# Performance work log

Measured on AMD Instinct MI355X. Metric: run time of the kernel, lower is better.

## Reference

```python
import jax, jax.numpy as jnp
import numpy as np

B, D = 8192, 1024

def setup_inputs() -> dict:
    key = jax.random.key(0)
    ks = jax.random.split(key, 5)
    scale = 1.0 / np.sqrt(D)
    return {
        "x": jax.random.normal(ks[0], (B, D), dtype=jnp.float32),
        "h": jax.random.normal(ks[1], (B, D), dtype=jnp.float32),
        "c": jax.random.normal(ks[2], (B, D), dtype=jnp.float32),
        # gate order: [input, forget, output, candidate]
        "Wx": jax.random.normal(ks[3], (4, D, D), dtype=jnp.float32) * scale,
        "Wh": jax.random.normal(ks[4], (4, D, D), dtype=jnp.float32) * scale,
    }

def reference(x, h, c, Wx, Wh):
    # two batched GEMMs covering all 8 projections: [B,D] x [4,D,D] -> [4,B,D]
    gx = jnp.einsum('bd,gdk->gbk', x, Wx)
    gh = jnp.einsum('bd,gdk->gbk', h, Wh)
    g = gx + gh
    i = jax.nn.sigmoid(g[0])
    f = jax.nn.sigmoid(g[1])
    o = jax.nn.sigmoid(g[2])
    u = jnp.tanh(g[3])
    c_t = i * u + f * c
    h_t = o * jnp.tanh(c_t)
    return (h_t, c_t)
```

## Files before the change

### kernel.cpp

```cpp
#include <hip/hip_runtime.h>
#include <hip/hip_bf16.h>
#include <cstdint>


#define LDS_TOTAL 131072

typedef __attribute__((ext_vector_type(8))) short bf16x8;
typedef __attribute__((ext_vector_type(16))) float f32x16;
typedef __attribute__((ext_vector_type(4))) unsigned int u32x4;

static __device__ __forceinline__ unsigned short f2bf(float f) {
  union { float f; unsigned int u; } v; v.f = f;
  unsigned int u = v.u;
  unsigned int r = (u + 0x7FFFu + ((u >> 16) & 1u)) >> 16;
  return (unsigned short)r;
}

static __device__ __forceinline__ void load16(const void* gp, void* lp) {
  __builtin_amdgcn_global_load_lds(
      (const __attribute__((address_space(1))) void*)gp,
      (__attribute__((address_space(3))) void*)lp, 16, 0, 0);
}

static __device__ __forceinline__ float sigmoid_f(float x) {
  return 1.0f / (1.0f + __expf(-x));
}
static __device__ __forceinline__ float tanh_f(float x) {
  float e = __expf(-2.0f * fabsf(x));
  float r = (1.0f - e) / (1.0f + e);
  return copysignf(r, x);
}

__global__ __launch_bounds__(256) void pack_a_kernel(
    const float* __restrict__ x, const float* __restrict__ h,
    unsigned short* __restrict__ Ap) {
  __shared__ float tile[64][65];
  const int b0 = (blockIdx.x >> 5) << 6;
  const int k0 = (blockIdx.x & 31) << 6;
  const float* src; int ks;
  if (k0 < 1024) { src = x; ks = k0; } else { src = h; ks = k0 - 1024; }
  const int r = threadIdx.x >> 4;
  const int c4 = (threadIdx.x & 15) << 2;
  #pragma unroll
  for (int s = 0; s < 4; ++s) {
    float4 v = *(const float4*)(src + (size_t)(b0 + s * 16 + r) * 1024 + ks + c4);
    tile[s * 16 + r][c4 + 0] = v.x; tile[s * 16 + r][c4 + 1] = v.y;
    tile[s * 16 + r][c4 + 2] = v.z; tile[s * 16 + r][c4 + 3] = v.w;
  }
  __syncthreads();
  #pragma unroll
  for (int i = 0; i < 2; ++i) {
    int cc = i * 256 + threadIdx.x;
    int kb = cc >> 6, bb = cc & 63;
    union { unsigned short s[8]; u32x4 v; } o;
    #pragma unroll
    for (int e = 0; e < 8; ++e) o.s[e] = f2bf(tile[bb][kb * 8 + e]);
    *(u32x4*)(Ap + ((size_t)((k0 >> 3) + kb) * 8192 + b0 + bb) * 8) = o.v;
  }
}

__global__ __launch_bounds__(256) void prep_w_kernel(
    const float* __restrict__ Wx, const float* __restrict__ Wh,
    unsigned short* __restrict__ Wt2) {
  __shared__ float tile[64][65];
  const int g = blockIdx.x >> 9;
  const int kt = (blockIdx.x >> 4) & 31;
  const int nt = blockIdx.x & 15;
  const int k0 = kt << 6, n0 = nt << 6;
  const float* W; int ks;
  if (k0 < 1024) { W = Wx + (size_t)g * 1048576; ks = k0; }
  else           { W = Wh + (size_t)g * 1048576; ks = k0 - 1024; }
  const int r = threadIdx.x >> 4;
  const int c4 = (threadIdx.x & 15) << 2;
  #pragma unroll
  for (int s = 0; s < 4; ++s) {
    float4 v = *(const float4*)(W + (size_t)(ks + s * 16 + r) * 1024 + n0 + c4);
    tile[s * 16 + r][c4 + 0] = v.x; tile[s * 16 + r][c4 + 1] = v.y;
    tile[s * 16 + r][c4 + 2] = v.z; tile[s * 16 + r][c4 + 3] = v.w;
  }
  __syncthreads();
  #pragma unroll
  for (int i = 0; i < 2; ++i) {
    int cc = i * 256 + threadIdx.x;
    int kb = cc >> 6, nn = cc & 63;
    union { unsigned short s[8]; u32x4 v; } o;
    #pragma unroll
    for (int e = 0; e < 8; ++e) o.s[e] = f2bf(tile[kb * 8 + e][nn]);
    *(u32x4*)(Wt2 + ((size_t)((k0 >> 3) + kb) * 4096 + g * 1024 + n0 + nn) * 8) = o.v;
  }
}

#define VMW(n) asm volatile("s_waitcnt vmcnt(" #n ")" ::: "memory")
#define LGKM0() asm volatile("s_waitcnt lgkmcnt(0)" ::: "memory")
#define BAR() __builtin_amdgcn_s_barrier()

__global__ __launch_bounds__(512, 2) void lstm_gemm_kernel(
    const unsigned short* __restrict__ Ap,
    const unsigned short* __restrict__ Wt2,
    const float* __restrict__ cprev,
    float* __restrict__ out) {
  extern __shared__ char lds[];
  const int tid = threadIdx.x;
  const int l = tid & 63;
  const int w = tid >> 6;
  const int wr = w >> 1;
  const int wc = w & 1;
  const int bid = blockIdx.x;
  const int xcd = bid & 7;
  const int cc = bid >> 3;
  const int nt = xcd * 2 + (cc >> 5);
  const int mt = cc & 31;
  const int m0 = mt << 8;
  const int n0 = nt << 6;

  char* const buf0 = lds;
  char* const buf1 = lds + 65536;

  f32x16 acc[2][4];
  #pragma unroll
  for (int mf = 0; mf < 2; ++mf)
    #pragma unroll
    for (int g = 0; g < 4; ++g) acc[mf][g] = (f32x16)0.0f;

  const int ln = l & 31;
  const int hl = l >> 5;

  const int aBase = hl * 4096 + (wr * 64 + ln) * 16;
  const int bBase = 32768 + hl * 1024 + (wc * 32 + ln) * 16;

  const unsigned short* const gA =
      Ap + (size_t)(tid >> 8) * 65536 + (size_t)(m0 + (tid & 255)) * 8;
  const unsigned short* const gB =
      Wt2 + (size_t)((tid >> 6) & 1) * 32768 +
      (size_t)((tid >> 7) * 1024 + n0 + (tid & 63)) * 8;
  const int dA = (tid & ~63) << 4;
  const int dB = 32768 + ((tid & ~63) << 4);

  auto stPair = [&](char* buf, int j, int t) {
    load16(gA + (size_t)(t * 8 + j * 2) * 65536, buf + j * 8192 + dA);
    load16(gB + (size_t)(t * 8 + j * 2) * 32768, buf + j * 8192 + dB);
  };

  bf16x8 a_[2][2], b_[2][4];
  auto rd2 = [&](const char* bufc, int h) {
    #pragma unroll
    for (int r = 0; r < 2; ++r) {
      const char* pb = bufc + (2 * h + r) * 8192;
      a_[r][0] = *(const bf16x8*)(pb + aBase);
      a_[r][1] = *(const bf16x8*)(pb + aBase + 512);
      b_[r][0] = *(const bf16x8*)(pb + bBase);
      b_[r][1] = *(const bf16x8*)(pb + bBase + 2048);
      b_[r][2] = *(const bf16x8*)(pb + bBase + 4096);
      b_[r][3] = *(const bf16x8*)(pb + bBase + 6144);
    }
  };
  auto mfma2 = [&]() {
    __builtin_amdgcn_s_setprio(1);
    #pragma unroll
    for (int r = 0; r < 2; ++r)
      #pragma unroll
      for (int mf = 0; mf < 2; ++mf)
        #pragma unroll
        for (int g = 0; g < 4; ++g)
          acc[mf][g] = __builtin_amdgcn_mfma_f32_32x32x16_bf16(
              a_[r][mf], b_[r][g], acc[mf][g], 0, 0, 0);
    __builtin_amdgcn_s_setprio(0);
  };

  #pragma unroll
  for (int j = 0; j < 4; ++j) stPair(buf0, j, 0);
  stPair(buf1, 0, 1); stPair(buf1, 1, 1);
  VMW(4);
  BAR();

  #pragma unroll 1
  for (int t = 0; t < 30; ++t) {
    char* bufc = lds + ((t & 1) << 16);
    char* bufn = lds + (((t + 1) & 1) << 16);
    rd2(bufc, 0);
    stPair(bufn, 2, t + 1); stPair(bufn, 3, t + 1);
    VMW(8); BAR(); LGKM0();
    mfma2();
    BAR();
    rd2(bufc, 1);
    stPair(bufc, 0, t + 2); stPair(bufc, 1, t + 2);
    VMW(8); BAR(); LGKM0();
    mfma2();
    BAR();
  }
  rd2(buf0, 0); stPair(buf1, 2, 31); stPair(buf1, 3, 31);
  VMW(8); BAR(); LGKM0(); mfma2(); BAR();
  rd2(buf0, 1);
  VMW(4); BAR(); LGKM0(); mfma2(); BAR();
  rd2(buf1, 0);
  VMW(0); BAR(); LGKM0(); mfma2(); BAR();
  rd2(buf1, 1);
  LGKM0(); mfma2();

  const int colB = n0 + wc * 32 + ln;
  #pragma unroll
  for (int mf = 0; mf < 2; ++mf) {
    #pragma unroll
    for (int r = 0; r < 16; ++r) {
      int row = m0 + wr * 64 + mf * 32 + (r & 3) + ((r >> 2) << 3) + (hl << 2);
      float gi = acc[mf][0][r];
      float gf = acc[mf][1][r];
      float go = acc[mf][2][r];
      float gu = acc[mf][3][r];
      float i_ = sigmoid_f(gi);
      float f_ = sigmoid_f(gf);
      float o_ = sigmoid_f(go);
      float u_ = tanh_f(gu);
      size_t idx = (size_t)row * 1024 + colB;
      float ct = i_ * u_ + f_ * cprev[idx];
      float ht = o_ * tanh_f(ct);
      out[idx] = ht;
      out[8388608 + idx] = ct;
    }
  }
}

extern "C" void kernel_launch(void* const* d_in, const int* in_sizes, int n_in,
                              void* d_out, int out_size, void* d_ws, size_t ws_size,
                              hipStream_t stream) {
  const float* x  = (const float*)d_in[0];
  const float* h  = (const float*)d_in[1];
  const float* c  = (const float*)d_in[2];
  const float* Wx = (const float*)d_in[3];
  const float* Wh = (const float*)d_in[4];
  float* out = (float*)d_out;

  unsigned short* Ap  = (unsigned short*)d_ws;
  unsigned short* Wt2 = (unsigned short*)((char*)d_ws + 33554432);

  hipFuncSetAttribute((const void*)lstm_gemm_kernel,
                      hipFuncAttributeMaxDynamicSharedMemorySize, LDS_TOTAL);

  pack_a_kernel<<<4096, 256, 0, stream>>>(x, h, Ap);
  prep_w_kernel<<<2048, 256, 0, stream>>>(Wx, Wh, Wt2);
  lstm_gemm_kernel<<<dim3(512), dim3(512), LDS_TOTAL, stream>>>(Ap, Wt2, c, out);
}
```

Before: 167.5 us.

## Fuse activation fp32-to-bf16 packing into GEMM mainloop, drop pack kernel

Removes the separate pack_a_kernel, which converted x and h to a bf16 K-blocked layout in workspace. The GEMM kernel now loads fp32 rows of x/h directly into registers, converts them to bf16 and writes them to LDS after the MFMA phase. This pipelines the register loads alongside the async B loads. It saves a full read and write pass over the 64MB of activations. In exchange the GEMM reads A as fp32, so A traffic doubles, and each M-tile's A is re-read by all 16 N-tile blocks. It also adds VALU conversion work, register pressure and possible LDS write bank conflicts in the mainloop.

```diff
diff --git a/kernel.cpp b/kernel.cpp
--- a/kernel.cpp
+++ b/kernel.cpp
@@ -29,34 +29,6 @@
   float e = __expf(-2.0f * fabsf(x));
   float r = (1.0f - e) / (1.0f + e);
   return copysignf(r, x);
-}
-
-__global__ __launch_bounds__(256) void pack_a_kernel(
-    const float* __restrict__ x, const float* __restrict__ h,
-    unsigned short* __restrict__ Ap) {
-  __shared__ float tile[64][65];
-  const int b0 = (blockIdx.x >> 5) << 6;
-  const int k0 = (blockIdx.x & 31) << 6;
-  const float* src; int ks;
-  if (k0 < 1024) { src = x; ks = k0; } else { src = h; ks = k0 - 1024; }
-  const int r = threadIdx.x >> 4;
-  const int c4 = (threadIdx.x & 15) << 2;
-  #pragma unroll
-  for (int s = 0; s < 4; ++s) {
-    float4 v = *(const float4*)(src + (size_t)(b0 + s * 16 + r) * 1024 + ks + c4);
-    tile[s * 16 + r][c4 + 0] = v.x; tile[s * 16 + r][c4 + 1] = v.y;
-    tile[s * 16 + r][c4 + 2] = v.z; tile[s * 16 + r][c4 + 3] = v.w;
-  }
-  __syncthreads();
-  #pragma unroll
-  for (int i = 0; i < 2; ++i) {
-    int cc = i * 256 + threadIdx.x;
-    int kb = cc >> 6, bb = cc & 63;
-    union { unsigned short s[8]; u32x4 v; } o;
-    #pragma unroll
-    for (int e = 0; e < 8; ++e) o.s[e] = f2bf(tile[bb][kb * 8 + e]);
-    *(u32x4*)(Ap + ((size_t)((k0 >> 3) + kb) * 8192 + b0 + bb) * 8) = o.v;
-  }
 }
 
 __global__ __launch_bounds__(256) void prep_w_kernel(
@@ -95,7 +67,8 @@
 #define BAR() __builtin_amdgcn_s_barrier()
 
 __global__ __launch_bounds__(512, 2) void lstm_gemm_kernel(
-    const unsigned short* __restrict__ Ap,
+    const float* __restrict__ x,
+    const float* __restrict__ hin,
     const unsigned short* __restrict__ Wt2,
     const float* __restrict__ cprev,
     float* __restrict__ out) {
@@ -128,17 +101,28 @@
   const int aBase = hl * 4096 + (wr * 64 + ln) * 16;
   const int bBase = 32768 + hl * 1024 + (wc * 32 + ln) * 16;
 
-  const unsigned short* const gA =
-      Ap + (size_t)(tid >> 8) * 65536 + (size_t)(m0 + (tid & 255)) * 8;
   const unsigned short* const gB =
       Wt2 + (size_t)((tid >> 6) & 1) * 32768 +
       (size_t)((tid >> 7) * 1024 + n0 + (tid & 63)) * 8;
-  const int dA = (tid & ~63) << 4;
   const int dB = 32768 + ((tid & ~63) << 4);
-
-  auto stPair = [&](char* buf, int j, int t) {
-    load16(gA + (size_t)(t * 8 + j * 2) * 65536, buf + j * 8192 + dA);
+  auto stB = [&](char* buf, int j, int t) {
     load16(gB + (size_t)(t * 8 + j * 2) * 32768, buf + j * 8192 + dB);
+  };
+
+  const int khalf = tid >> 8;
+  const float* const xrow = x   + (size_t)(m0 + (tid & 255)) * 1024;
+  const float* const hrow = hin + (size_t)(m0 + (tid & 255)) * 1024;
+  auto ldA = [&](int j, int t, float4& v0, float4& v1) {
+    const int kk = ((t * 8 + j * 2 + khalf) * 8) & 1023;
+    const float* p = ((t < 16) ? xrow : hrow) + kk;
+    v0 = ((const float4*)p)[0];
+    v1 = ((const float4*)p)[1];
+  };
+  auto wrA = [&](char* buf, int j, const float4& v0, const float4& v1) {
+    union { unsigned short s[8]; u32x4 u; } o;
+    o.s[0] = f2bf(v0.x); o.s[1] = f2bf(v0.y); o.s[2] = f2bf(v0.z); o.s[3] = f2bf(v0.w);
+    o.s[4] = f2bf(v1.x); o.s[5] = f2bf(v1.y); o.s[6] = f2bf(v1.z); o.s[7] = f2bf(v1.w);
+    *(u32x4*)(buf + j * 8192 + (tid << 4)) = o.u;
   };
 
   bf16x8 a_[2][2], b_[2][4];
@@ -168,30 +152,54 @@
   };
 
   #pragma unroll
-  for (int j = 0; j < 4; ++j) stPair(buf0, j, 0);
-  stPair(buf1, 0, 1); stPair(buf1, 1, 1);
-  VMW(4);
+  for (int j = 0; j < 4; ++j) stB(buf0, j, 0);
+  stB(buf1, 0, 1); stB(buf1, 1, 1);
+  {
+    float4 u0, u1;
+    #pragma unroll
+    for (int j = 0; j < 4; ++j) { ldA(j, 0, u0, u1); wrA(buf0, j, u0, u1); }
+    ldA(0, 1, u0, u1); wrA(buf1, 0, u0, u1);
+    ldA(1, 1, u0, u1); wrA(buf1, 1, u0, u1);
+  }
+  LGKM0();
+  VMW(2);
   BAR();
 
   #pragma unroll 1
   for (int t = 0; t < 30; ++t) {
     char* bufc = lds + ((t & 1) << 16);
     char* bufn = lds + (((t + 1) & 1) << 16);
+    float4 p0a, p0b, p1a, p1b;
+    ldA(2, t + 1, p0a, p0b); ldA(3, t + 1, p1a, p1b);
     rd2(bufc, 0);
-    stPair(bufn, 2, t + 1); stPair(bufn, 3, t + 1);
+    stB(bufn, 2, t + 1); stB(bufn, 3, t + 1);
     VMW(8); BAR(); LGKM0();
     mfma2();
+    __builtin_amdgcn_sched_barrier(0);
+    wrA(bufn, 2, p0a, p0b); wrA(bufn, 3, p1a, p1b);
     BAR();
+    ldA(0, t + 2, p0a, p0b); ldA(1, t + 2, p1a, p1b);
     rd2(bufc, 1);
-    stPair(bufc, 0, t + 2); stPair(bufc, 1, t + 2);
+    stB(bufc, 0, t + 2); stB(bufc, 1, t + 2);
     VMW(8); BAR(); LGKM0();
     mfma2();
+    __builtin_amdgcn_sched_barrier(0);
+    wrA(bufc, 0, p0a, p0b); wrA(bufc, 1, p1a, p1b);
     BAR();
   }
-  rd2(buf0, 0); stPair(buf1, 2, 31); stPair(buf1, 3, 31);
-  VMW(8); BAR(); LGKM0(); mfma2(); BAR();
+  {
+    float4 p0a, p0b, p1a, p1b;
+    ldA(2, 31, p0a, p0b); ldA(3, 31, p1a, p1b);
+    rd2(buf0, 0);
+    stB(buf1, 2, 31); stB(buf1, 3, 31);
+    VMW(8); BAR(); LGKM0();
+    mfma2();
+    __builtin_amdgcn_sched_barrier(0);
+    wrA(buf1, 2, p0a, p0b); wrA(buf1, 3, p1a, p1b);
+    BAR();
+  }
   rd2(buf0, 1);
-  VMW(4); BAR(); LGKM0(); mfma2(); BAR();
+  VMW(2); BAR(); LGKM0(); mfma2(); BAR();
   rd2(buf1, 0);
   VMW(0); BAR(); LGKM0(); mfma2(); BAR();
   rd2(buf1, 1);
@@ -230,13 +238,11 @@
   const float* Wh = (const float*)d_in[4];
   float* out = (float*)d_out;
 
-  unsigned short* Ap  = (unsigned short*)d_ws;
-  unsigned short* Wt2 = (unsigned short*)((char*)d_ws + 33554432);
+  unsigned short* Wt2 = (unsigned short*)d_ws;
 
   hipFuncSetAttribute((const void*)lstm_gemm_kernel,
                       hipFuncAttributeMaxDynamicSharedMemorySize, LDS_TOTAL);
 
-  pack_a_kernel<<<4096, 256, 0, stream>>>(x, h, Ap);
   prep_w_kernel<<<2048, 256, 0, stream>>>(Wx, Wh, Wt2);
-  lstm_gemm_kernel<<<dim3(512), dim3(512), LDS_TOTAL, stream>>>(Ap, Wt2, c, out);
-}
+  lstm_gemm_kernel<<<dim3(512), dim3(512), LDS_TOTAL, stream>>>(x, h, Wt2, c, out);
+}
```

Result: slower. 322.5 us (+92.5%).
